# Kernel optimization log

Hardware: AMD Instinct MI355X
Metric: run time of the kernel (lower is better)

Reference implementation:

```python
import jax, jax.numpy as jnp
import numpy as np

B, N = 4, 512
D_MODEL, ATOM_CH = 256, 5
PAIR_H, N_RBF, RBF_MAX = 128, 16, 4.0
LN_EPS = 1e-5


def setup_inputs() -> dict:
    key = jax.random.key(0)
    ks = jax.random.split(key, 12)
    sd = 1.0 / np.sqrt(D_MODEL)
    sh = 1.0 / np.sqrt(PAIR_H)
    return {
        "trunk_out": jax.random.normal(ks[0], (B, N, D_MODEL), jnp.float32),
        "coords": jax.random.normal(ks[1], (B, N, 3), jnp.float32),
        "pad_mask": jax.random.randint(ks[2], (B, N), 0, 2).astype(bool),
        "ln_g": jnp.ones((D_MODEL,), jnp.float32),
        "ln_b": jnp.zeros((D_MODEL,), jnp.float32),
        "w_a1": jax.random.normal(ks[3], (D_MODEL, D_MODEL), jnp.float32) * sd,
        "b_a1": jnp.zeros((D_MODEL,), jnp.float32),
        "w_a2": jax.random.normal(ks[4], (D_MODEL, ATOM_CH), jnp.float32) * sd,
        "b_a2": jnp.zeros((ATOM_CH,), jnp.float32),
        "w_pi": jax.random.normal(ks[5], (D_MODEL, PAIR_H), jnp.float32) * sd,
        "w_pj": jax.random.normal(ks[6], (D_MODEL, PAIR_H), jnp.float32) * sd,
        "w_pr": jax.random.normal(ks[7], (N_RBF, PAIR_H), jnp.float32) * 0.25,
        "b_p1": jnp.zeros((PAIR_H,), jnp.float32),
        "w_p2": jax.random.normal(ks[8], (PAIR_H,), jnp.float32) * sh,
        "b_p2": jnp.zeros((1,), jnp.float32),
    }


def _forward(trunk_out, coords, pad_mask, ln_g, ln_b, w_a1, b_a1, w_a2, b_a2,
             w_pi, w_pj, w_pr, b_p1, w_p2, b_p2):
    dt = trunk_out.dtype
    valid = ~pad_mask                                   # (B, N)
    validf = valid.astype(dt)

    # ---- atom head: LayerNorm -> Linear -> SiLU -> Linear, pad-masked ----
    mu = trunk_out.mean(-1, keepdims=True)
    var = jnp.mean((trunk_out - mu) ** 2, -1, keepdims=True)
    xn = (trunk_out - mu) * jax.lax.rsqrt(var + LN_EPS) * ln_g + ln_b
    atom_delta = jax.nn.silu(xn @ w_a1 + b_a1) @ w_a2 + b_a2
    atom_delta = jnp.where(pad_mask[..., None], jnp.zeros((), dt), atom_delta)

    # ---- geometry features (non-periodic adapter) ----
    delta = coords[:, :, None, :] - coords[:, None, :, :]   # (B, N, N, 3)
    sq = jnp.sum(delta * delta, -1)
    dist = jnp.sqrt(jnp.maximum(sq, 1e-12))                 # safe sqrt (diag)
    centers = jnp.linspace(0.0, RBF_MAX, N_RBF, dtype=dt)
    gamma = jnp.asarray(1.0 / (RBF_MAX / max(N_RBF - 1, 1)) ** 2, dt)
    rbf = jnp.exp(-gamma * (dist[..., None] - centers) ** 2)  # (B, N, N, R)
    pair_mask = valid[:, :, None] & valid[:, None, :]

    # ---- pair head: LazyLinear on cat([hi, hj, rbf]) == sum of 3 projections ----
    pi = jnp.einsum('bid,dh->bih', trunk_out, w_pi)         # (B, N, H)
    pj = jnp.einsum('bjd,dh->bjh', trunk_out, w_pj)
    h1 = jax.nn.silu(pi[:, :, None, :] + pj[:, None, :, :]
                     + jnp.einsum('bijr,rh->bijh', rbf, w_pr) + b_p1)
    pw = jnp.einsum('bijh,h->bij', h1, w_p2) + b_p2[0]      # (B, N, N)
    pw = jnp.where(pair_mask, pw, jnp.zeros((), dt))
    pw = jnp.where(jnp.eye(N, dtype=bool), jnp.zeros((), dt), pw)  # zero diag

    # ---- weighted-sum coordinate update ----
    coord_delta = jnp.einsum('bij,bijc->bic', pw, delta)    # (B, N, 3)
    denom = jnp.maximum(validf.sum(1, keepdims=True), 1.0)  # (B, 1)
    coord_delta = coord_delta / denom[..., None]
    coord_delta = jnp.where(pad_mask[..., None], jnp.zeros((), dt), coord_delta)
    mean = (coord_delta * validf[..., None]).sum(1, keepdims=True) / denom[..., None]
    coord_delta = jnp.where(pad_mask[..., None], jnp.zeros((), dt), coord_delta - mean)
    return atom_delta, coord_delta


def reference(trunk_out, coords, pad_mask, ln_g, ln_b, w_a1, b_a1, w_a2, b_a2,
              w_pi, w_pj, w_pr, b_p1, w_p2, b_p2):
    return _forward(trunk_out, coords, pad_mask, ln_g, ln_b, w_a1, b_a1,
                    w_a2, b_a2, w_pi, w_pj, w_pr, b_p1, w_p2, b_p2)
```

## Files before the change

### kernel.cpp

```cpp
#include <hip/hip_runtime.h>
#include <hip/hip_bf16.h>

#define BN 2048
#define NSEQ 512
#define D 256
#define H 128
#define R 16
#define AC 5
#define CHUNK 128
#define ROWG 8
#define SPLIT 4

using bf16 = __hip_bfloat16;

__device__ __forceinline__ float fast_silu(float t) {
    const float e = __expf(-t);
    return t * __builtin_amdgcn_rcpf(1.0f + e);
}
__device__ __forceinline__ float bf2f(unsigned short u) {
    return __uint_as_float(((unsigned)u) << 16);
}
__device__ __forceinline__ unsigned short f2bu(float v) {
    const bf16 pb = __float2bfloat16(v);
    return *(const unsigned short*)&pb;
}

__global__ __launch_bounds__(256) void batch_kernel(
    const int* __restrict__ pad, const float* __restrict__ coords,
    int* __restrict__ jlist_g, int* __restrict__ M_g, float* __restrict__ csum_g)
{
    const int b = blockIdx.x;
    const int tid = threadIdx.x;
    __shared__ int s_wcnt[8];
    __shared__ int s_wbase[8];
    __shared__ float r1[256], r2[256], r3[256];
    const int wv = tid >> 6, lane = tid & 63;
    unsigned long long bm[2];
    float sx = 0.0f, sy = 0.0f, sz = 0.0f;
    #pragma unroll
    for (int cc = 0; cc < 2; ++cc) {
        const int j = cc * 256 + tid;
        const int ok = (pad[b * NSEQ + j] == 0);
        bm[cc] = __ballot(ok);
        if (lane == 0) s_wcnt[cc * 4 + wv] = __popcll(bm[cc]);
        if (ok) {
            sx += coords[(size_t)(b * NSEQ + j) * 3 + 0];
            sy += coords[(size_t)(b * NSEQ + j) * 3 + 1];
            sz += coords[(size_t)(b * NSEQ + j) * 3 + 2];
        }
    }
    r1[tid] = sx; r2[tid] = sy; r3[tid] = sz;
    __syncthreads();
    for (int s = 128; s > 0; s >>= 1) {
        if (tid < s) { r1[tid] += r1[tid + s]; r2[tid] += r2[tid + s]; r3[tid] += r3[tid + s]; }
        __syncthreads();
    }
    if (tid == 0) {
        int acc = 0;
        #pragma unroll
        for (int q = 0; q < 8; ++q) { s_wbase[q] = acc; acc += s_wcnt[q]; }
        M_g[b] = acc;
        csum_g[b * 3 + 0] = r1[0];
        csum_g[b * 3 + 1] = r2[0];
        csum_g[b * 3 + 2] = r3[0];
    }
    __syncthreads();
    #pragma unroll
    for (int cc = 0; cc < 2; ++cc) {
        const int j = cc * 256 + tid;
        if (pad[b * NSEQ + j] == 0) {
            const int pos = s_wbase[cc * 4 + wv]
                          + __popcll(bm[cc] & ((1ull << lane) - 1ull));
            jlist_g[b * NSEQ + pos] = j;
        }
    }
}

__global__ __launch_bounds__(512) void row_kernel(
    const float* __restrict__ trunk, const int* __restrict__ pad,
    const float* __restrict__ ln_g, const float* __restrict__ ln_b,
    const float* __restrict__ w_a1, const float* __restrict__ b_a1,
    const float* __restrict__ w_a2, const float* __restrict__ b_a2,
    const float* __restrict__ w_pi, const float* __restrict__ w_pj,
    const float* __restrict__ b_p1,
    float* __restrict__ out_atom, unsigned short* __restrict__ pj_o,
    unsigned short* __restrict__ pib_o)
{
    const int row0 = blockIdx.x * ROWG;
    const int tid = threadIdx.x;
    const int wv = tid >> 6, lane = tid & 63;
    __shared__ __align__(16) float x_t[2][D][4];
    __shared__ __align__(16) float xn_t[2][D][4];
    __shared__ float y[ROWG][D];
    __shared__ float mu_s[ROWG], rs_s[ROWG];

    #pragma unroll
    for (int gg = 0; gg < 4; ++gg) {
        const int g = gg * 2 + (tid >> 8);
        const int e = tid & 255;
        x_t[g >> 2][e][g & 3] = trunk[(size_t)(row0 + g) * D + e];
    }
    __syncthreads();

    {
        const int g = wv;
        float s = 0.0f, ss = 0.0f;
        #pragma unroll
        for (int e2 = lane; e2 < D; e2 += 64) {
            const float v = x_t[g >> 2][e2][g & 3];
            s += v; ss += v * v;
        }
        #pragma unroll
        for (int off = 32; off; off >>= 1) {
            s  += __shfl_xor(s, off);
            ss += __shfl_xor(ss, off);
        }
        if (lane == 0) {
            const float mu  = s * (1.0f / D);
            const float var = ss * (1.0f / D) - mu * mu;
            mu_s[g] = mu;
            rs_s[g] = rsqrtf(var + 1e-5f);
        }
    }
    __syncthreads();
    #pragma unroll
    for (int gg = 0; gg < 4; ++gg) {
        const int g = gg * 2 + (tid >> 8);
        const int e = tid & 255;
        xn_t[g >> 2][e][g & 3] =
            (x_t[g >> 2][e][g & 3] - mu_s[g]) * rs_s[g] * ln_g[e] + ln_b[e];
    }
    __syncthreads();

    if (tid < 256) {
        const float bb = b_a1[tid];
        float a0 = bb, a1v = bb, a2v = bb, a3 = bb, a4 = bb, a5 = bb, a6 = bb, a7 = bb;
        for (int d = 0; d < D; ++d) {
            const float w = w_a1[d * D + tid];
            const float4 lo = *(const float4*)xn_t[0][d];
            const float4 hi = *(const float4*)xn_t[1][d];
            a0  = fmaf(lo.x, w, a0);  a1v = fmaf(lo.y, w, a1v);
            a2v = fmaf(lo.z, w, a2v); a3  = fmaf(lo.w, w, a3);
            a4  = fmaf(hi.x, w, a4);  a5  = fmaf(hi.y, w, a5);
            a6  = fmaf(hi.z, w, a6);  a7  = fmaf(hi.w, w, a7);
        }
        y[0][tid] = a0  / (1.0f + expf(-a0));
        y[1][tid] = a1v / (1.0f + expf(-a1v));
        y[2][tid] = a2v / (1.0f + expf(-a2v));
        y[3][tid] = a3  / (1.0f + expf(-a3));
        y[4][tid] = a4  / (1.0f + expf(-a4));
        y[5][tid] = a5  / (1.0f + expf(-a5));
        y[6][tid] = a6  / (1.0f + expf(-a6));
        y[7][tid] = a7  / (1.0f + expf(-a7));
    } else if (tid < 384) {
        const int h = tid - 256;
        float p0 = 0.f, p1 = 0.f, p2 = 0.f, p3 = 0.f, p4 = 0.f, p5 = 0.f, p6 = 0.f, p7 = 0.f;
        for (int d = 0; d < D; ++d) {
            const float w = w_pi[d * H + h];
            const float4 lo = *(const float4*)x_t[0][d];
            const float4 hi = *(const float4*)x_t[1][d];
            p0 = fmaf(lo.x, w, p0); p1 = fmaf(lo.y, w, p1);
            p2 = fmaf(lo.z, w, p2); p3 = fmaf(lo.w, w, p3);
            p4 = fmaf(hi.x, w, p4); p5 = fmaf(hi.y, w, p5);
            p6 = fmaf(hi.z, w, p6); p7 = fmaf(hi.w, w, p7);
        }
        const float bb = b_p1[h];
        const float pv[ROWG] = {p0 + bb, p1 + bb, p2 + bb, p3 + bb,
                                p4 + bb, p5 + bb, p6 + bb, p7 + bb};
        #pragma unroll
        for (int g = 0; g < ROWG; ++g)
            pib_o[(size_t)(row0 + g) * H + h] = f2bu(pv[g]);
    } else {
        const int h = tid - 384;
        float p0 = 0.f, p1 = 0.f, p2 = 0.f, p3 = 0.f, p4 = 0.f, p5 = 0.f, p6 = 0.f, p7 = 0.f;
        for (int d = 0; d < D; ++d) {
            const float w = w_pj[d * H + h];
            const float4 lo = *(const float4*)x_t[0][d];
            const float4 hi = *(const float4*)x_t[1][d];
            p0 = fmaf(lo.x, w, p0); p1 = fmaf(lo.y, w, p1);
            p2 = fmaf(lo.z, w, p2); p3 = fmaf(lo.w, w, p3);
            p4 = fmaf(hi.x, w, p4); p5 = fmaf(hi.y, w, p5);
            p6 = fmaf(hi.z, w, p6); p7 = fmaf(hi.w, w, p7);
        }
        const float pv[ROWG] = {p0, p1, p2, p3, p4, p5, p6, p7};
        #pragma unroll
        for (int g = 0; g < ROWG; ++g)
            pj_o[(size_t)(row0 + g) * H + h] = f2bu(pv[g]);
    }
    __syncthreads();

    if (tid < ROWG * AC) {
        const int g = tid / AC, c = tid % AC;
        float a = b_a2[c];
        for (int d = 0; d < D; ++d) a = fmaf(y[g][d], w_a2[d * AC + c], a);
        out_atom[(row0 + g) * AC + c] = (pad[row0 + g] != 0) ? 0.0f : a;
    }
}

__device__ __forceinline__ void pair_body(
    const float pvx, const float pvy,
    const float* __restrict__ rbf_row, const float4 dk,
    const float pibx, const float piby,
    const float* wprA, const float* wprB, const float2 wp22,
    float& cdx, float& cdy, float& cdz)
{
    float t0a = pibx + pvx, t0b = 0.0f;
    float t1a = piby + pvy, t1b = 0.0f;
    #pragma unroll
    for (int r = 0; r < R; r += 2) {
        const float qa = rbf_row[r];
        const float qb = rbf_row[r + 1];
        t0a = fmaf(qa, wprA[r],     t0a);
        t0b = fmaf(qb, wprA[r + 1], t0b);
        t1a = fmaf(qa, wprB[r],     t1a);
        t1b = fmaf(qb, wprB[r + 1], t1b);
    }
    const float u0 = fast_silu(t0a + t0b);
    const float u1 = fast_silu(t1a + t1b);
    const float part = u0 * wp22.x + u1 * wp22.y;
    cdx = fmaf(part, dk.x, cdx);
    cdy = fmaf(part, dk.y, cdy);
    cdz = fmaf(part, dk.z, cdz);
}

__global__ __launch_bounds__(256) void pair_kernel(
    const float* __restrict__ coords, const int* __restrict__ pad,
    const float* __restrict__ w_pr, const float* __restrict__ w_p2,
    const unsigned short* __restrict__ pj_i, const unsigned short* __restrict__ pib_i,
    const int* __restrict__ jlist_g, const int* __restrict__ M_g,
    float* __restrict__ cd_part)
{
    const int row  = blockIdx.x >> 2;
    const int part_id = blockIdx.x & 3;
    const int b = row >> 9;
    const int tid = threadIdx.x;

    if (pad[row] != 0) {
        if (tid == 0) {
            cd_part[(row * SPLIT + part_id) * 3 + 0] = 0.0f;
            cd_part[(row * SPLIT + part_id) * 3 + 1] = 0.0f;
            cd_part[(row * SPLIT + part_id) * 3 + 2] = 0.0f;
        }
        return;
    }

    __shared__ __align__(16) float s_rbf[CHUNK][20];
    __shared__ __align__(16) float4 s_d4[CHUNK];
    __shared__ int   s_jl[CHUNK];
    __shared__ float rw1[4], rw2[4], rw3[4];

    const int wv = tid >> 6, lane = tid & 63;
    const int M = M_g[b];
    const int Mq  = (M + SPLIT - 1) / SPLIT;
    const int kLo = part_id * Mq;
    const int kHi = min(M, kLo + Mq);

    float wprA[R], wprB[R];
    #pragma unroll
    for (int r = 0; r < R; ++r) {
        const float2 wv2 = ((const float2*)(w_pr + r * H))[lane];
        wprA[r] = wv2.x;
        wprB[r] = wv2.y;
    }
    const ushort2 pibu = ((const ushort2*)(pib_i + (size_t)row * H))[lane];
    const float pibx = bf2f(pibu.x), piby = bf2f(pibu.y);
    const float2 wp22 = ((const float2*)w_p2)[lane];
    const float cix = coords[(size_t)row * 3 + 0];
    const float ciy = coords[(size_t)row * 3 + 1];
    const float ciz = coords[(size_t)row * 3 + 2];

    float cdx = 0.0f, cdy = 0.0f, cdz = 0.0f;
    const unsigned short* pjb = pj_i + (size_t)b * NSEQ * H;
    const float gamma = 14.0625f;

    for (int c0 = kLo; c0 < kHi; c0 += CHUNK) {
        const int cn = (kHi - c0 < CHUNK) ? (kHi - c0) : CHUNK;
        __syncthreads();
        if (tid < cn) {
            const int j = jlist_g[b * NSEQ + c0 + tid];
            s_jl[tid] = j;
            const float* cj = coords + (size_t)(b * NSEQ + j) * 3;
            const float dx = cix - cj[0];
            const float dy = ciy - cj[1];
            const float dz = ciz - cj[2];
            const float sq = dx * dx + dy * dy + dz * dz;
            const float dist = sqrtf(fmaxf(sq, 1e-12f));
            s_d4[tid] = make_float4(dx, dy, dz, 0.0f);
            #pragma unroll
            for (int c = 0; c < 4; ++c) {
                float4 q;
                const float t0 = dist - (float)(4.0 * (4 * c + 0) / 15.0);
                const float t1 = dist - (float)(4.0 * (4 * c + 1) / 15.0);
                const float t2 = dist - (float)(4.0 * (4 * c + 2) / 15.0);
                const float t3 = dist - (float)(4.0 * (4 * c + 3) / 15.0);
                q.x = __expf(-gamma * t0 * t0);
                q.y = __expf(-gamma * t1 * t1);
                q.z = __expf(-gamma * t2 * t2);
                q.w = __expf(-gamma * t3 * t3);
                *(float4*)(&s_rbf[tid][4 * c]) = q;
            }
        }
        __syncthreads();

        const int cl = cn - 1;
        int k = wv;
        ushort2 pv0 = ((const ushort2*)(pjb + (size_t)s_jl[min(k,      cl)] * H))[lane];
        ushort2 pv1 = ((const ushort2*)(pjb + (size_t)s_jl[min(k + 4,  cl)] * H))[lane];
        ushort2 pv2 = ((const ushort2*)(pjb + (size_t)s_jl[min(k + 8,  cl)] * H))[lane];
        ushort2 pv3 = ((const ushort2*)(pjb + (size_t)s_jl[min(k + 12, cl)] * H))[lane];
        for (; k < cn; k += 16) {
            const int kn = k + 16;
            const ushort2 nv0 = ((const ushort2*)(pjb + (size_t)s_jl[min(kn,      cl)] * H))[lane];
            const ushort2 nv1 = ((const ushort2*)(pjb + (size_t)s_jl[min(kn + 4,  cl)] * H))[lane];
            const ushort2 nv2 = ((const ushort2*)(pjb + (size_t)s_jl[min(kn + 8,  cl)] * H))[lane];
            const ushort2 nv3 = ((const ushort2*)(pjb + (size_t)s_jl[min(kn + 12, cl)] * H))[lane];

            const int k1 = k + 4, k2 = k + 8, k3 = k + 12;
            pair_body(bf2f(pv0.x), bf2f(pv0.y), s_rbf[k], s_d4[k], pibx, piby,
                      wprA, wprB, wp22, cdx, cdy, cdz);
            if (k1 < cn) pair_body(bf2f(pv1.x), bf2f(pv1.y), s_rbf[k1], s_d4[k1], pibx, piby,
                                   wprA, wprB, wp22, cdx, cdy, cdz);
            if (k2 < cn) pair_body(bf2f(pv2.x), bf2f(pv2.y), s_rbf[k2], s_d4[k2], pibx, piby,
                                   wprA, wprB, wp22, cdx, cdy, cdz);
            if (k3 < cn) pair_body(bf2f(pv3.x), bf2f(pv3.y), s_rbf[k3], s_d4[k3], pibx, piby,
                                   wprA, wprB, wp22, cdx, cdy, cdz);
            pv0 = nv0; pv1 = nv1; pv2 = nv2; pv3 = nv3;
        }
    }
    #pragma unroll
    for (int off = 32; off; off >>= 1) {
        cdx += __shfl_xor(cdx, off);
        cdy += __shfl_xor(cdy, off);
        cdz += __shfl_xor(cdz, off);
    }
    if (lane == 0) { rw1[wv] = cdx; rw2[wv] = cdy; rw3[wv] = cdz; }
    __syncthreads();
    if (tid == 0) {
        cd_part[(row * SPLIT + part_id) * 3 + 0] = rw1[0] + rw1[1] + rw1[2] + rw1[3];
        cd_part[(row * SPLIT + part_id) * 3 + 1] = rw2[0] + rw2[1] + rw2[2] + rw2[3];
        cd_part[(row * SPLIT + part_id) * 3 + 2] = rw3[0] + rw3[1] + rw3[2] + rw3[3];
    }
}

__global__ __launch_bounds__(256) void finalize_kernel(
    const float* __restrict__ cd_part, const int* __restrict__ pad,
    const float* __restrict__ coords, const int* __restrict__ M_g,
    const float* __restrict__ csum_g, const float* __restrict__ b_p2,
    float* __restrict__ out_coord)
{
    const int b = blockIdx.x;
    const int tid = threadIdx.x;
    __shared__ float r1[256], r2[256], r3[256];
    const float bp2 = b_p2[0];
    const float Mf  = (float)M_g[b];
    const float csx = csum_g[b * 3 + 0];
    const float csy = csum_g[b * 3 + 1];
    const float csz = csum_g[b * 3 + 2];

    float sx = 0.0f, sy = 0.0f, sz = 0.0f;
    for (int ii = tid; ii < NSEQ; ii += 256) {
        const int row = b * NSEQ + ii;
        if (pad[row] == 0) {
            float cx = bp2 * fmaf(Mf, coords[(size_t)row * 3 + 0], -csx);
            float cy = bp2 * fmaf(Mf, coords[(size_t)row * 3 + 1], -csy);
            float cz = bp2 * fmaf(Mf, coords[(size_t)row * 3 + 2], -csz);
            #pragma unroll
            for (int q = 0; q < SPLIT; ++q) {
                cx += cd_part[(row * SPLIT + q) * 3 + 0];
                cy += cd_part[(row * SPLIT + q) * 3 + 1];
                cz += cd_part[(row * SPLIT + q) * 3 + 2];
            }
            sx += cx; sy += cy; sz += cz;
        }
    }
    r1[tid] = sx; r2[tid] = sy; r3[tid] = sz;
    __syncthreads();
    for (int s = 128; s > 0; s >>= 1) {
        if (tid < s) { r1[tid] += r1[tid + s]; r2[tid] += r2[tid + s]; r3[tid] += r3[tid + s]; }
        __syncthreads();
    }
    const float denom = fmaxf(Mf, 1.0f);
    const float inv_d = 1.0f / denom;
    const float mx = r1[0] * inv_d * inv_d;
    const float my = r2[0] * inv_d * inv_d;
    const float mz = r3[0] * inv_d * inv_d;
    for (int ii = tid; ii < NSEQ; ii += 256) {
        const int row = b * NSEQ + ii;
        if (pad[row] == 0) {
            float cx = bp2 * fmaf(Mf, coords[(size_t)row * 3 + 0], -csx);
            float cy = bp2 * fmaf(Mf, coords[(size_t)row * 3 + 1], -csy);
            float cz = bp2 * fmaf(Mf, coords[(size_t)row * 3 + 2], -csz);
            #pragma unroll
            for (int q = 0; q < SPLIT; ++q) {
                cx += cd_part[(row * SPLIT + q) * 3 + 0];
                cy += cd_part[(row * SPLIT + q) * 3 + 1];
                cz += cd_part[(row * SPLIT + q) * 3 + 2];
            }
            out_coord[row * 3 + 0] = cx * inv_d - mx;
            out_coord[row * 3 + 1] = cy * inv_d - my;
            out_coord[row * 3 + 2] = cz * inv_d - mz;
        } else {
            out_coord[row * 3 + 0] = 0.0f;
            out_coord[row * 3 + 1] = 0.0f;
            out_coord[row * 3 + 2] = 0.0f;
        }
    }
}

extern "C" void kernel_launch(void* const* d_in, const int* in_sizes, int n_in,
                              void* d_out, int out_size, void* d_ws, size_t ws_size,
                              hipStream_t stream) {
    const float* trunk  = (const float*)d_in[0];
    const float* coords = (const float*)d_in[1];
    const int*   pad    = (const int*)d_in[2];
    const float* ln_g   = (const float*)d_in[3];
    const float* ln_b   = (const float*)d_in[4];
    const float* w_a1   = (const float*)d_in[5];
    const float* b_a1   = (const float*)d_in[6];
    const float* w_a2   = (const float*)d_in[7];
    const float* b_a2   = (const float*)d_in[8];
    const float* w_pi   = (const float*)d_in[9];
    const float* w_pj   = (const float*)d_in[10];
    const float* w_pr   = (const float*)d_in[11];
    const float* b_p1   = (const float*)d_in[12];
    const float* w_p2   = (const float*)d_in[13];
    const float* b_p2   = (const float*)d_in[14];

    float* out_atom  = (float*)d_out;
    float* out_coord = out_atom + (size_t)BN * AC;

    int*   jlist_g = (int*)d_ws;
    int*   M_g     = jlist_g + 4 * NSEQ;
    float* csum_g  = (float*)(M_g + 16);
    float* cd_part = csum_g + 16;
    unsigned short* pj_buf  = (unsigned short*)(cd_part + (size_t)BN * SPLIT * 3);
    unsigned short* pib_buf = pj_buf + (size_t)BN * H;

    batch_kernel<<<4, 256, 0, stream>>>(pad, coords, jlist_g, M_g, csum_g);
    row_kernel<<<BN / ROWG, 512, 0, stream>>>(trunk, pad, ln_g, ln_b, w_a1, b_a1,
                                              w_a2, b_a2, w_pi, w_pj, b_p1,
                                              out_atom, pj_buf, pib_buf);
    pair_kernel<<<BN * SPLIT, 256, 0, stream>>>(coords, pad, w_pr, w_p2,
                                                pj_buf, pib_buf, jlist_g, M_g, cd_part);
    finalize_kernel<<<4, 256, 0, stream>>>(cd_part, pad, coords, M_g, csum_g,
                                           b_p2, out_coord);
}
```

Baseline: 66.43 us.

## Make pair kernel persistent with atomic work-queue scheduling

Launches a fixed grid of 2048 blocks that repeatedly take (row, split) work items from a global atomic counter, instead of launching one block per item. The counter is reset in the batch kernel. The aim is to cut block launch overhead and the cost of reloading the w_pr/w_p2 registers for every item, and to balance work around padded rows. In exchange, every item now costs an atomic and two extra block-wide syncs.

```diff
diff --git a/kernel.cpp b/kernel.cpp
--- a/kernel.cpp
+++ b/kernel.cpp
@@ -10,6 +10,7 @@
 #define CHUNK 128
 #define ROWG 8
 #define SPLIT 4
+#define NPERS 2048
 
 using bf16 = __hip_bfloat16;
 
@@ -27,10 +28,12 @@
 
 __global__ __launch_bounds__(256) void batch_kernel(
     const int* __restrict__ pad, const float* __restrict__ coords,
-    int* __restrict__ jlist_g, int* __restrict__ M_g, float* __restrict__ csum_g)
+    int* __restrict__ jlist_g, int* __restrict__ M_g, float* __restrict__ csum_g,
+    int* __restrict__ counter)
 {
     const int b = blockIdx.x;
     const int tid = threadIdx.x;
+    if (b == 0 && tid == 0) counter[0] = 0;
     __shared__ int s_wcnt[8];
     __shared__ int s_wbase[8];
     __shared__ float r1[256], r2[256], r3[256];
@@ -228,32 +231,17 @@
     const float* __restrict__ w_pr, const float* __restrict__ w_p2,
     const unsigned short* __restrict__ pj_i, const unsigned short* __restrict__ pib_i,
     const int* __restrict__ jlist_g, const int* __restrict__ M_g,
+    int* __restrict__ counter,
     float* __restrict__ cd_part)
 {
-    const int row  = blockIdx.x >> 2;
-    const int part_id = blockIdx.x & 3;
-    const int b = row >> 9;
     const int tid = threadIdx.x;
-
-    if (pad[row] != 0) {
-        if (tid == 0) {
-            cd_part[(row * SPLIT + part_id) * 3 + 0] = 0.0f;
-            cd_part[(row * SPLIT + part_id) * 3 + 1] = 0.0f;
-            cd_part[(row * SPLIT + part_id) * 3 + 2] = 0.0f;
-        }
-        return;
-    }
+    const int wv = tid >> 6, lane = tid & 63;
 
     __shared__ __align__(16) float s_rbf[CHUNK][20];
     __shared__ __align__(16) float4 s_d4[CHUNK];
     __shared__ int   s_jl[CHUNK];
     __shared__ float rw1[4], rw2[4], rw3[4];
-
-    const int wv = tid >> 6, lane = tid & 63;
-    const int M = M_g[b];
-    const int Mq  = (M + SPLIT - 1) / SPLIT;
-    const int kLo = part_id * Mq;
-    const int kHi = min(M, kLo + Mq);
+    __shared__ int   s_item;
 
     float wprA[R], wprB[R];
     #pragma unroll
@@ -262,83 +250,110 @@
         wprA[r] = wv2.x;
         wprB[r] = wv2.y;
     }
-    const ushort2 pibu = ((const ushort2*)(pib_i + (size_t)row * H))[lane];
-    const float pibx = bf2f(pibu.x), piby = bf2f(pibu.y);
     const float2 wp22 = ((const float2*)w_p2)[lane];
-    const float cix = coords[(size_t)row * 3 + 0];
-    const float ciy = coords[(size_t)row * 3 + 1];
-    const float ciz = coords[(size_t)row * 3 + 2];
-
-    float cdx = 0.0f, cdy = 0.0f, cdz = 0.0f;
-    const unsigned short* pjb = pj_i + (size_t)b * NSEQ * H;
     const float gamma = 14.0625f;
 
-    for (int c0 = kLo; c0 < kHi; c0 += CHUNK) {
-        const int cn = (kHi - c0 < CHUNK) ? (kHi - c0) : CHUNK;
+    for (;;) {
         __syncthreads();
-        if (tid < cn) {
-            const int j = jlist_g[b * NSEQ + c0 + tid];
-            s_jl[tid] = j;
-            const float* cj = coords + (size_t)(b * NSEQ + j) * 3;
-            const float dx = cix - cj[0];
-            const float dy = ciy - cj[1];
-            const float dz = ciz - cj[2];
-            const float sq = dx * dx + dy * dy + dz * dz;
-            const float dist = sqrtf(fmaxf(sq, 1e-12f));
-            s_d4[tid] = make_float4(dx, dy, dz, 0.0f);
-            #pragma unroll
-            for (int c = 0; c < 4; ++c) {
-                float4 q;
-                const float t0 = dist - (float)(4.0 * (4 * c + 0) / 15.0);
-                const float t1 = dist - (float)(4.0 * (4 * c + 1) / 15.0);
-                const float t2 = dist - (float)(4.0 * (4 * c + 2) / 15.0);
-                const float t3 = dist - (float)(4.0 * (4 * c + 3) / 15.0);
-                q.x = __expf(-gamma * t0 * t0);
-                q.y = __expf(-gamma * t1 * t1);
-                q.z = __expf(-gamma * t2 * t2);
-                q.w = __expf(-gamma * t3 * t3);
-                *(float4*)(&s_rbf[tid][4 * c]) = q;
+        if (tid == 0) s_item = atomicAdd(counter, 1);
+        __syncthreads();
+        const int item = s_item;
+        if (item >= BN * SPLIT) break;
+
+        const int row = item >> 2;
+        const int part_id = item & 3;
+        const int b = row >> 9;
+
+        if (pad[row] != 0) {
+            if (tid == 0) {
+                cd_part[(row * SPLIT + part_id) * 3 + 0] = 0.0f;
+                cd_part[(row * SPLIT + part_id) * 3 + 1] = 0.0f;
+                cd_part[(row * SPLIT + part_id) * 3 + 2] = 0.0f;
             }
-        }
+            continue;
+        }
+
+        const int M = M_g[b];
+        const int Mq  = (M + SPLIT - 1) / SPLIT;
+        const int kLo = part_id * Mq;
+        const int kHi = min(M, kLo + Mq);
+
+        const ushort2 pibu = ((const ushort2*)(pib_i + (size_t)row * H))[lane];
+        const float pibx = bf2f(pibu.x), piby = bf2f(pibu.y);
+        const float cix = coords[(size_t)row * 3 + 0];
+        const float ciy = coords[(size_t)row * 3 + 1];
+        const float ciz = coords[(size_t)row * 3 + 2];
+        const unsigned short* pjb = pj_i + (size_t)b * NSEQ * H;
+
+        float cdx = 0.0f, cdy = 0.0f, cdz = 0.0f;
+
+        for (int c0 = kLo; c0 < kHi; c0 += CHUNK) {
+            const int cn = (kHi - c0 < CHUNK) ? (kHi - c0) : CHUNK;
+            __syncthreads();
+            if (tid < cn) {
+                const int j = jlist_g[b * NSEQ + c0 + tid];
+                s_jl[tid] = j;
+                const float* cj = coords + (size_t)(b * NSEQ + j) * 3;
+                const float dx = cix - cj[0];
+                const float dy = ciy - cj[1];
+                const float dz = ciz - cj[2];
+                const float sq = dx * dx + dy * dy + dz * dz;
+                const float dist = sqrtf(fmaxf(sq, 1e-12f));
+                s_d4[tid] = make_float4(dx, dy, dz, 0.0f);
+                #pragma unroll
+                for (int c = 0; c < 4; ++c) {
+                    float4 q;
+                    const float t0 = dist - (float)(4.0 * (4 * c + 0) / 15.0);
+                    const float t1 = dist - (float)(4.0 * (4 * c + 1) / 15.0);
+                    const float t2 = dist - (float)(4.0 * (4 * c + 2) / 15.0);
+                    const float t3 = dist - (float)(4.0 * (4 * c + 3) / 15.0);
+                    q.x = __expf(-gamma * t0 * t0);
+                    q.y = __expf(-gamma * t1 * t1);
+                    q.z = __expf(-gamma * t2 * t2);
+                    q.w = __expf(-gamma * t3 * t3);
+                    *(float4*)(&s_rbf[tid][4 * c]) = q;
+                }
+            }
+            __syncthreads();
+
+            const int cl = cn - 1;
+            int k = wv;
+            ushort2 pv0 = ((const ushort2*)(pjb + (size_t)s_jl[min(k,      cl)] * H))[lane];
+            ushort2 pv1 = ((const ushort2*)(pjb + (size_t)s_jl[min(k + 4,  cl)] * H))[lane];
+            ushort2 pv2 = ((const ushort2*)(pjb + (size_t)s_jl[min(k + 8,  cl)] * H))[lane];
+            ushort2 pv3 = ((const ushort2*)(pjb + (size_t)s_jl[min(k + 12, cl)] * H))[lane];
+            for (; k < cn; k += 16) {
+                const int kn = k + 16;
+                const ushort2 nv0 = ((const ushort2*)(pjb + (size_t)s_jl[min(kn,      cl)] * H))[lane];
+                const ushort2 nv1 = ((const ushort2*)(pjb + (size_t)s_jl[min(kn + 4,  cl)] * H))[lane];
+                const ushort2 nv2 = ((const ushort2*)(pjb + (size_t)s_jl[min(kn + 8,  cl)] * H))[lane];
+                const ushort2 nv3 = ((const ushort2*)(pjb + (size_t)s_jl[min(kn + 12, cl)] * H))[lane];
+
+                const int k1 = k + 4, k2 = k + 8, k3 = k + 12;
+                pair_body(bf2f(pv0.x), bf2f(pv0.y), s_rbf[k], s_d4[k], pibx, piby,
+                          wprA, wprB, wp22, cdx, cdy, cdz);
+                if (k1 < cn) pair_body(bf2f(pv1.x), bf2f(pv1.y), s_rbf[k1], s_d4[k1], pibx, piby,
+                                       wprA, wprB, wp22, cdx, cdy, cdz);
+                if (k2 < cn) pair_body(bf2f(pv2.x), bf2f(pv2.y), s_rbf[k2], s_d4[k2], pibx, piby,
+                                       wprA, wprB, wp22, cdx, cdy, cdz);
+                if (k3 < cn) pair_body(bf2f(pv3.x), bf2f(pv3.y), s_rbf[k3], s_d4[k3], pibx, piby,
+                                       wprA, wprB, wp22, cdx, cdy, cdz);
+                pv0 = nv0; pv1 = nv1; pv2 = nv2; pv3 = nv3;
+            }
+        }
+        #pragma unroll
+        for (int off = 32; off; off >>= 1) {
+            cdx += __shfl_xor(cdx, off);
+            cdy += __shfl_xor(cdy, off);
+            cdz += __shfl_xor(cdz, off);
+        }
+        if (lane == 0) { rw1[wv] = cdx; rw2[wv] = cdy; rw3[wv] = cdz; }
         __syncthreads();
-
-        const int cl = cn - 1;
-        int k = wv;
-        ushort2 pv0 = ((const ushort2*)(pjb + (size_t)s_jl[min(k,      cl)] * H))[lane];
-        ushort2 pv1 = ((const ushort2*)(pjb + (size_t)s_jl[min(k + 4,  cl)] * H))[lane];
-        ushort2 pv2 = ((const ushort2*)(pjb + (size_t)s_jl[min(k + 8,  cl)] * H))[lane];
-        ushort2 pv3 = ((const ushort2*)(pjb + (size_t)s_jl[min(k + 12, cl)] * H))[lane];
-        for (; k < cn; k += 16) {
-            const int kn = k + 16;
-            const ushort2 nv0 = ((const ushort2*)(pjb + (size_t)s_jl[min(kn,      cl)] * H))[lane];
-            const ushort2 nv1 = ((const ushort2*)(pjb + (size_t)s_jl[min(kn + 4,  cl)] * H))[lane];
-            const ushort2 nv2 = ((const ushort2*)(pjb + (size_t)s_jl[min(kn + 8,  cl)] * H))[lane];
-            const ushort2 nv3 = ((const ushort2*)(pjb + (size_t)s_jl[min(kn + 12, cl)] * H))[lane];
-
-            const int k1 = k + 4, k2 = k + 8, k3 = k + 12;
-            pair_body(bf2f(pv0.x), bf2f(pv0.y), s_rbf[k], s_d4[k], pibx, piby,
-                      wprA, wprB, wp22, cdx, cdy, cdz);
-            if (k1 < cn) pair_body(bf2f(pv1.x), bf2f(pv1.y), s_rbf[k1], s_d4[k1], pibx, piby,
-                                   wprA, wprB, wp22, cdx, cdy, cdz);
-            if (k2 < cn) pair_body(bf2f(pv2.x), bf2f(pv2.y), s_rbf[k2], s_d4[k2], pibx, piby,
-                                   wprA, wprB, wp22, cdx, cdy, cdz);
-            if (k3 < cn) pair_body(bf2f(pv3.x), bf2f(pv3.y), s_rbf[k3], s_d4[k3], pibx, piby,
-                                   wprA, wprB, wp22, cdx, cdy, cdz);
-            pv0 = nv0; pv1 = nv1; pv2 = nv2; pv3 = nv3;
-        }
-    }
-    #pragma unroll
-    for (int off = 32; off; off >>= 1) {
-        cdx += __shfl_xor(cdx, off);
-        cdy += __shfl_xor(cdy, off);
-        cdz += __shfl_xor(cdz, off);
-    }
-    if (lane == 0) { rw1[wv] = cdx; rw2[wv] = cdy; rw3[wv] = cdz; }
-    __syncthreads();
-    if (tid == 0) {
-        cd_part[(row * SPLIT + part_id) * 3 + 0] = rw1[0] + rw1[1] + rw1[2] + rw1[3];
-        cd_part[(row * SPLIT + part_id) * 3 + 1] = rw2[0] + rw2[1] + rw2[2] + rw2[3];
-        cd_part[(row * SPLIT + part_id) * 3 + 2] = rw3[0] + rw3[1] + rw3[2] + rw3[3];
+        if (tid == 0) {
+            cd_part[(row * SPLIT + part_id) * 3 + 0] = rw1[0] + rw1[1] + rw1[2] + rw1[3];
+            cd_part[(row * SPLIT + part_id) * 3 + 1] = rw2[0] + rw2[1] + rw2[2] + rw2[3];
+            cd_part[(row * SPLIT + part_id) * 3 + 2] = rw3[0] + rw3[1] + rw3[2] + rw3[3];
+        }
     }
 }
 
@@ -432,16 +447,18 @@
     int*   jlist_g = (int*)d_ws;
     int*   M_g     = jlist_g + 4 * NSEQ;
     float* csum_g  = (float*)(M_g + 16);
-    float* cd_part = csum_g + 16;
+    int*   counter = (int*)(csum_g + 16);
+    float* cd_part = (float*)(counter + 16);
     unsigned short* pj_buf  = (unsigned short*)(cd_part + (size_t)BN * SPLIT * 3);
     unsigned short* pib_buf = pj_buf + (size_t)BN * H;
 
-    batch_kernel<<<4, 256, 0, stream>>>(pad, coords, jlist_g, M_g, csum_g);
+    batch_kernel<<<4, 256, 0, stream>>>(pad, coords, jlist_g, M_g, csum_g, counter);
     row_kernel<<<BN / ROWG, 512, 0, stream>>>(trunk, pad, ln_g, ln_b, w_a1, b_a1,
                                               w_a2, b_a2, w_pi, w_pj, b_p1,
                                               out_atom, pj_buf, pib_buf);
-    pair_kernel<<<BN * SPLIT, 256, 0, stream>>>(coords, pad, w_pr, w_p2,
-                                                pj_buf, pib_buf, jlist_g, M_g, cd_part);
+    pair_kernel<<<NPERS, 256, 0, stream>>>(coords, pad, w_pr, w_p2,
+                                           pj_buf, pib_buf, jlist_g, M_g,
+                                           counter, cd_part);
     finalize_kernel<<<4, 256, 0, stream>>>(cd_part, pad, coords, M_g, csum_g,
                                            b_p2, out_coord);
 }
```

Result: slower. 152.2 us (+129.2%).
